# Kernel tuning notes

Measured on AMD Instinct MI355X. Metric: run time of the kernel, lower is better.

## Reference

```python
import jax, jax.numpy as jnp
import numpy as np

DEPTH, DIM, DH, H, DQ, V = 4, 1024, 4096, 8, 128, 32000
B, L = 2, 1024


def setup_inputs() -> dict:
    key = jax.random.key(0)
    ks = iter(jax.random.split(key, 48))
    def nrm(shape, scale=1.0):
        return jax.random.normal(next(ks), shape, jnp.float32) * scale
    d = {}
    d["x"] = nrm((B, L, V))
    d["tin_w"] = nrm((DIM, V), V ** -0.5)
    d["tin_b"] = nrm((DIM,), 0.02)
    d["tout_w"] = nrm((V, DIM), DIM ** -0.5)
    d["tout_b"] = nrm((V,), 0.02)
    d["wq_w"] = nrm((DEPTH, H * DQ, DIM), DIM ** -0.5)
    d["wq_b"] = nrm((DEPTH, H * DQ), 0.02)
    d["wk_w"] = nrm((DEPTH, H * DQ, DIM), DIM ** -0.5)
    d["wk_b"] = nrm((DEPTH, H * DQ), 0.02)
    d["wv_w"] = nrm((DEPTH, H * DQ, DIM), DIM ** -0.5)
    d["wv_b"] = nrm((DEPTH, H * DQ), 0.02)
    d["wo_w"] = nrm((DEPTH, DIM, H * DQ), (H * DQ) ** -0.5)
    d["wo_b"] = nrm((DEPTH, DIM), 0.02)
    d["f1_w"] = nrm((DEPTH, DH, DIM), DIM ** -0.5)
    d["f1_b"] = nrm((DEPTH, DH), 0.02)
    d["f2_w"] = nrm((DEPTH, DIM, DH), DH ** -0.5)
    d["f2_b"] = nrm((DEPTH, DIM), 0.02)
    d["phz_re"] = nrm((DEPTH, H, DQ))
    d["phz_im"] = nrm((DEPTH, H, DQ))
    d["amp"] = nrm((DEPTH, H))
    d["lc_re"] = nrm((DEPTH, H, DQ, DQ), 0.02)
    d["lc_im"] = nrm((DEPTH, H, DQ, DQ), 0.02)
    return d


def _layernorm(x):
    m = x.mean(-1, keepdims=True)
    v = ((x - m) ** 2).mean(-1, keepdims=True)
    return (x - m) * jax.lax.rsqrt(v + 1e-5)


def _retention(x, qw, qb, kw, kb, vw, vb, ow, ob, pre, pim, amp, lcr, lci):
    b, l, _ = x.shape
    q = (x @ qw.T + qb).reshape(b, l, H, DQ)
    k = (x @ kw.T + kb).reshape(b, l, H, DQ)
    v = (x @ vw.T + vb).reshape(b, l, H, DQ)
    pz = pre + 1j * pim                              # [H,DQ] complex
    phase = pz / jnp.abs(pz)                         # unit modulus
    a = jax.nn.sigmoid(amp)                          # [H]
    phazor = phase * a[:, None]
    n = jnp.arange(l)
    pp = phase[None, :, :] ** n[:, None, None]       # [L,H,DQ]
    pp_inv = phase[None, :, :] ** (-n)[:, None, None]
    php = phazor[None, :, :] ** n[:, None, None]
    lc = jax.lax.stop_gradient(lcr + 1j * lci)       # [H,DQ,DQ], detached in torch
    qc = q.astype(jnp.complex64)
    kc = k.astype(jnp.complex64)
    vc = v.astype(jnp.complex64)
    cross = jnp.einsum('blhd,lhd,hde->blhe', qc, php * phazor[None], lc)
    tril = n[:, None] >= n[None, :]
    expn = jnp.where(tril, n[:, None] - n[None, :], 0)           # [L,L]
    mask = jnp.where(tril[None], a[:, None, None] ** expn[None], 0.0)  # [H,L,L]
    qk = jnp.einsum('blhd,bmhd->bhlm', qc * pp[None], kc * pp_inv[None])
    inner = jnp.einsum('bhlm,bmhd->blhd', qk * mask[None].astype(jnp.complex64), vc)
    y = jax.nn.silu((inner + cross).real).reshape(b, l, H * DQ)
    return y @ ow.T + ob


def reference(x, tin_w, tin_b, tout_w, tout_b, wq_w, wq_b, wk_w, wk_b, wv_w, wv_b,
              wo_w, wo_b, f1_w, f1_b, f2_w, f2_b, phz_re, phz_im, amp, lc_re, lc_im):
    h = x @ tin_w.T + tin_b
    for i in range(DEPTH):
        r = _retention(_layernorm(h), wq_w[i], wq_b[i], wk_w[i], wk_b[i],
                       wv_w[i], wv_b[i], wo_w[i], wo_b[i],
                       phz_re[i], phz_im[i], amp[i], lc_re[i], lc_im[i])
        h = h + r
        f = _layernorm(h)
        f = jax.nn.silu(f @ f1_w[i].T + f1_b[i]) @ f2_w[i].T + f2_b[i]
        h = h + f
    return h @ tout_w.T + tout_b
```

## Files before the change

kernel.cpp:

```cpp
#include <hip/hip_runtime.h>
#include <hip/hip_bf16.h>
#include <stdint.h>

#define DEPTH 4
#define DIM   1024
#define DH    4096
#define NH    8
#define DQ    128
#define VOC   32000
#define BATCH 2
#define SEQ   1024
#define ROWS  (BATCH*SEQ)

#define PQKV  ((long long)ROWS*DIM)
#define PQKV3 ((long long)ROWS*3*DIM)
#define PROT  ((long long)BATCH*NH*SEQ*2*DQ)
#define PVT   ((long long)BATCH*NH*DQ*SEQ)
#define PS    ((long long)BATCH*NH*SEQ*SEQ)
#define PMID  ((long long)ROWS*DH)
#define PY    ((long long)ROWS*DIM)
#define PLC   ((long long)NH*DQ*2*DQ)

typedef __hip_bfloat16 bf16;
using f32x4  = __attribute__((ext_vector_type(4))) float;
using bf16x8 = __attribute__((ext_vector_type(8))) __bf16;

__device__ __forceinline__ void wpair(bf16* p, long long off, long long plane, float v) {
  bf16 hi = __float2bfloat16(v);
  p[off] = hi;
  p[off + plane] = __float2bfloat16(v - __bfloat162float(hi));
}

__device__ __forceinline__ void gload_lds16(const void* g, void* l) {
  __builtin_amdgcn_global_load_lds(
      (const __attribute__((address_space(1))) void*)g,
      (__attribute__((address_space(3))) void*)(uintptr_t)l,
      16, 0, 0);
}

#define BM 128
#define BN 128
#define BKK 64
#define PL 16384

template<int EPI, int SA, int SB>
__global__ __launch_bounds__(256, (SA || SB) ? 2 : 4)
void gemm_bt(const bf16* __restrict__ A, long long sA, long long pA, int lda,
             const bf16* __restrict__ B, long long sB, long long pB, int ldb, int bmod,
             void* __restrict__ Cv, long long sC, long long pC, int ldc,
             const float* __restrict__ bias, int hmod,
             int M, int N, int K, int ksplit)
{
  __shared__ int4 sbuf[1024 * (2 + SA + SB)];
  char* Asb = (char*)sbuf;
  char* Bsb = Asb + PL * (1 + SA);

  const int tid  = threadIdx.x;
  const int lane = tid & 63;
  const int wave = tid >> 6;
  const int wr   = wave >> 1;
  const int wc   = wave & 1;
  const int z    = blockIdx.z;
  const int zb   = z / ksplit;
  const int ks   = z - zb * ksplit;
  const int Kc   = K / ksplit;
  const int k0   = ks * Kc;
  const long long tm = (long long)blockIdx.x * BM;
  const long long tn = (long long)blockIdx.y * BN;

  const bf16* Ab = A + (long long)zb * sA;
  const bf16* Bb = B + (long long)(zb % bmod) * sB;

  f32x4 acc[4][4] = {};

  for (int kt = k0; kt < k0 + Kc; kt += BKK) {
#pragma unroll
    for (int j = 0; j < 4; ++j) {
      int slot0 = j*256 + wave*64;
      int i = slot0 + lane;
      int row = i >> 3;
      int gc  = (i & 7) ^ (row & 7);
      long long ga = (tm + row) * (long long)lda + kt + gc*8;
      long long gb = (tn + row) * (long long)ldb + kt + gc*8;
      gload_lds16(Ab + ga, Asb + slot0*16);
      if (SA) gload_lds16(Ab + pA + ga, Asb + PL + slot0*16);
      gload_lds16(Bb + gb, Bsb + slot0*16);
      if (SB) gload_lds16(Bb + pB + gb, Bsb + PL + slot0*16);
    }
    __syncthreads();
#pragma unroll
    for (int kh = 0; kh < 2; ++kh) {
      const int cb = kh*4 + (lane >> 4);
      int4 avh[4], bvh[4], avl[4], bvl[4];
#pragma unroll
      for (int mi = 0; mi < 4; ++mi) {
        int m = wr*64 + mi*16 + (lane & 15);
        int off = m*128 + ((cb ^ (m & 7)) << 4);
        avh[mi] = *(const int4*)(Asb + off);
        if (SA) avl[mi] = *(const int4*)(Asb + PL + off);
      }
#pragma unroll
      for (int nj = 0; nj < 4; ++nj) {
        int n = wc*64 + nj*16 + (lane & 15);
        int off = n*128 + ((cb ^ (n & 7)) << 4);
        bvh[nj] = *(const int4*)(Bsb + off);
        if (SB) bvl[nj] = *(const int4*)(Bsb + PL + off);
      }
#pragma unroll
      for (int mi = 0; mi < 4; ++mi)
#pragma unroll
        for (int nj = 0; nj < 4; ++nj)
          acc[mi][nj] = __builtin_amdgcn_mfma_f32_16x16x32_bf16(
              __builtin_bit_cast(bf16x8, avh[mi]),
              __builtin_bit_cast(bf16x8, bvh[nj]), acc[mi][nj], 0, 0, 0);
      if (SA)
#pragma unroll
        for (int mi = 0; mi < 4; ++mi)
#pragma unroll
          for (int nj = 0; nj < 4; ++nj)
            acc[mi][nj] = __builtin_amdgcn_mfma_f32_16x16x32_bf16(
                __builtin_bit_cast(bf16x8, avl[mi]),
                __builtin_bit_cast(bf16x8, bvh[nj]), acc[mi][nj], 0, 0, 0);
      if (SB)
#pragma unroll
        for (int mi = 0; mi < 4; ++mi)
#pragma unroll
          for (int nj = 0; nj < 4; ++nj)
            acc[mi][nj] = __builtin_amdgcn_mfma_f32_16x16x32_bf16(
                __builtin_bit_cast(bf16x8, avh[mi]),
                __builtin_bit_cast(bf16x8, bvl[nj]), acc[mi][nj], 0, 0, 0);
    }
    __syncthreads();
  }

  const float* dtab = (EPI == 7) ? bias + (zb % hmod) * (SEQ + 1) : nullptr;
  const int col = lane & 15;
  const int rb  = (lane >> 4) << 2;
  float* Cf = (float*)Cv + (long long)zb * sC;
  bf16*  Ch = (bf16*) Cv + (long long)zb * sC;

#pragma unroll
  for (int mi = 0; mi < 4; ++mi)
#pragma unroll
    for (int nj = 0; nj < 4; ++nj) {
      long long gn = tn + wc*64 + nj*16 + col;
      float bv_ = (EPI != 7 && bias && ks == 0) ? bias[gn] : 0.f;
#pragma unroll
      for (int r = 0; r < 4; ++r) {
        long long gm = tm + wr*64 + mi*16 + rb + r;
        float v = acc[mi][nj][r] + bv_;
        long long off = gm * (long long)ldc + gn;
        if (EPI == 0)      Cf[off] = v;
        else if (EPI == 3) { if (ksplit > 1) atomicAdd(&Cf[off], v); else Cf[off] += v; }
        else if (EPI == 5) wpair(Ch, off, pC, v);
        else if (EPI == 6) wpair(Ch, off, pC, v / (1.f + __expf(-v)));
        else {
          long long dlt = gm - gn;
          float dcy = (dlt >= 0) ? dtab[dlt] : 0.f;
          Ch[off] = __float2bfloat16(acc[mi][nj][r] * dcy);
        }
      }
    }
}

__global__ void zero_kernel(float4* __restrict__ p, long long n4) {
  long long i = (long long)blockIdx.x * blockDim.x + threadIdx.x;
  if (i < n4) p[i] = float4{0.f, 0.f, 0.f, 0.f};
}

__global__ void cast_kernel(const float* __restrict__ in,
                            bf16* __restrict__ out, long long n4) {
  long long i = (long long)blockIdx.x * blockDim.x + threadIdx.x;
  if (i >= n4) return;
  float4 v = ((const float4*)in)[i];
  bf16 a = __float2bfloat16(v.x), b = __float2bfloat16(v.y);
  bf16 c = __float2bfloat16(v.z), d = __float2bfloat16(v.w);
  ushort4 o{__builtin_bit_cast(unsigned short, a), __builtin_bit_cast(unsigned short, b),
            __builtin_bit_cast(unsigned short, c), __builtin_bit_cast(unsigned short, d)};
  ((ushort4*)out)[i] = o;
}

__global__ void cast_pair_kernel(const float* __restrict__ in,
                                 bf16* __restrict__ hi, bf16* __restrict__ lo,
                                 long long n) {
  long long i = (long long)blockIdx.x * blockDim.x + threadIdx.x;
  if (i >= n) return;
  float v = in[i];
  bf16 h = __float2bfloat16(v);
  hi[i] = h;
  lo[i] = __float2bfloat16(v - __bfloat162float(h));
}

__global__ void bias3_kernel(const float* __restrict__ q, const float* __restrict__ k,
                             const float* __restrict__ v, float* __restrict__ o) {
  int i = blockIdx.x * blockDim.x + threadIdx.x;
  if (i < DIM) o[i] = q[i];
  else if (i < 2*DIM) o[i] = k[i - DIM];
  else if (i < 3*DIM) o[i] = v[i - 2*DIM];
}

__global__ void decay_kernel(const float* __restrict__ amp, float* __restrict__ dtab) {
  const int h = blockIdx.x, n = threadIdx.x;
  const float a = 1.f / (1.f + __expf(-amp[h]));
  for (int i = n; i <= SEQ; i += blockDim.x)
    dtab[h*(SEQ+1) + i] = powf(a, (float)i);
}

__global__ void ln_kernel(const float* __restrict__ in, bf16* __restrict__ out) {
  const int row = blockIdx.x;
  const int tid = threadIdx.x;
  const float4 v = ((const float4*)(in + (size_t)row*DIM))[tid];
  float s  = v.x + v.y + v.z + v.w;
  float s2 = v.x*v.x + v.y*v.y + v.z*v.z + v.w*v.w;
#pragma unroll
  for (int o = 32; o > 0; o >>= 1) { s += __shfl_xor(s, o); s2 += __shfl_xor(s2, o); }
  __shared__ float red[8];
  const int wv = tid >> 6;
  if ((tid & 63) == 0) { red[wv] = s; red[4 + wv] = s2; }
  __syncthreads();
  s  = red[0] + red[1] + red[2] + red[3];
  s2 = red[4] + red[5] + red[6] + red[7];
  const float mean = s * (1.f / DIM);
  const float var  = s2 * (1.f / DIM) - mean * mean;
  const float inv  = rsqrtf(var + 1e-5f);
  long long base = (long long)row*DIM + tid*4;
  wpair(out, base + 0, PQKV, (v.x - mean) * inv);
  wpair(out, base + 1, PQKV, (v.y - mean) * inv);
  wpair(out, base + 2, PQKV, (v.z - mean) * inv);
  wpair(out, base + 3, PQKV, (v.w - mean) * inv);
}

__global__ void rotate_kernel(const bf16* __restrict__ qkv,
                              const float* __restrict__ pre, const float* __restrict__ pim,
                              const float* __restrict__ dtab,
                              bf16* __restrict__ qrot, bf16* __restrict__ krot,
                              bf16* __restrict__ qwb) {
  const int d = threadIdx.x, l = blockIdx.x, h = blockIdx.y, b = blockIdx.z;
  const float tr = pre[h*DQ + d], ti = pim[h*DQ + d];
  const float theta = atan2f(ti, tr);
  const long long rowb = (long long)(b*SEQ + l)*(3*DIM) + h*DQ + d;
  const float qv = __bfloat162float(qkv[rowb]) + __bfloat162float(qkv[rowb + PQKV3]);
  const float kv = __bfloat162float(qkv[rowb + DIM]) + __bfloat162float(qkv[rowb + DIM + PQKV3]);
  float sn, cs;
  sincosf(theta * (float)l, &sn, &cs);
  const long long dst = ((long long)(b*NH + h)*SEQ + l)*(2*DQ) + d;
  qrot[dst]      = __float2bfloat16(qv * cs);
  qrot[dst + DQ] = __float2bfloat16(qv * sn);
  krot[dst]      = __float2bfloat16(kv * cs);
  krot[dst + DQ] = __float2bfloat16(kv * sn);
  float sn2, cs2;
  sincosf(theta * (float)(l + 1), &sn2, &cs2);
  const float ad = dtab[h*(SEQ+1) + l + 1];
  qwb[dst]      = __float2bfloat16(qv * ad * cs2);
  qwb[dst + DQ] = __float2bfloat16(qv * ad * sn2);
}

__global__ void vt_kernel(const bf16* __restrict__ qkv, bf16* __restrict__ vt) {
  __shared__ float tile[64][65];
  const int t  = threadIdx.x;
  const int c  = t & 63, r4 = t >> 6;
  const int m0 = blockIdx.x * 64;
  const int d0 = blockIdx.y * 64;
  const int h  = blockIdx.z & (NH - 1);
  const int b  = blockIdx.z >> 3;
#pragma unroll
  for (int rr = 0; rr < 64; rr += 4) {
    const int m = m0 + rr + r4;
    const long long src = (long long)(b*SEQ + m)*(3*DIM) + 2*DIM + h*DQ + d0 + c;
    tile[rr + r4][c] = __bfloat162float(qkv[src]) + __bfloat162float(qkv[src + PQKV3]);
  }
  __syncthreads();
#pragma unroll
  for (int rr = 0; rr < 64; rr += 4) {
    const int d = rr + r4;
    vt[((long long)(b*NH + h)*DQ + d0 + d)*SEQ + m0 + c] = __float2bfloat16(tile[c][d]);
  }
}

__global__ void siluret_kernel(const float* __restrict__ ret, bf16* __restrict__ y) {
  const int d = threadIdx.x, l = blockIdx.x, h = blockIdx.y, b = blockIdx.z;
  float r = ret[((long long)(b*NH + h)*SEQ + l)*DQ + d];
  float s = r / (1.f + __expf(-r));
  wpair(y, ((long long)(b*SEQ + l)*NH + h)*DQ + d, PY, s);
}

__global__ void lccat_kernel(const float* __restrict__ lcr, const float* __restrict__ lci,
                             bf16* __restrict__ lc) {
  const int d = threadIdx.x, e = blockIdx.x, h = blockIdx.y;
  float vr = lcr[((long long)h*DQ + d)*DQ + e];
  float vi = lci[((long long)h*DQ + d)*DQ + e];
  long long dst = ((long long)h*DQ + e)*(2*DQ) + d;
  lc[dst]      = __float2bfloat16(vr);
  lc[dst + DQ] = __float2bfloat16(-vi);
}

extern "C" void kernel_launch(void* const* d_in, const int* in_sizes, int n_in,
                              void* d_out, int out_size, void* d_ws, size_t ws_size,
                              hipStream_t stream) {
  const float* x      = (const float*)d_in[0];
  const float* tin_w  = (const float*)d_in[1];
  const float* tin_b  = (const float*)d_in[2];
  const float* tout_w = (const float*)d_in[3];
  const float* tout_b = (const float*)d_in[4];
  const float* wq_w   = (const float*)d_in[5];
  const float* wq_b   = (const float*)d_in[6];
  const float* wk_w   = (const float*)d_in[7];
  const float* wk_b   = (const float*)d_in[8];
  const float* wv_w   = (const float*)d_in[9];
  const float* wv_b   = (const float*)d_in[10];
  const float* wo_w   = (const float*)d_in[11];
  const float* wo_b   = (const float*)d_in[12];
  const float* f1_w   = (const float*)d_in[13];
  const float* f1_b   = (const float*)d_in[14];
  const float* f2_w   = (const float*)d_in[15];
  const float* f2_b   = (const float*)d_in[16];
  const float* phz_re = (const float*)d_in[17];
  const float* phz_im = (const float*)d_in[18];
  const float* amp    = (const float*)d_in[19];
  const float* lc_re  = (const float*)d_in[20];
  const float* lc_im  = (const float*)d_in[21];
  (void)in_sizes; (void)n_in; (void)out_size; (void)ws_size;

  char* w = (char*)d_ws;
  auto alloc = [&](size_t bytes) {
    char* p = w; w += (bytes + 255) & ~(size_t)255; return p;
  };
  auto palloc = [&](long long elems) {
    return (bf16*)alloc((size_t)elems * 2 * 2);
  };

  const long long WP = 3LL*DIM*DIM;
  float* h     = (float*)alloc((size_t)ROWS*DIM*4);
  float* ret   = (float*)alloc((size_t)BATCH*NH*SEQ*DQ*4);
  float* qkvbi = (float*)alloc((size_t)3*DIM*4);
  float* dtab  = (float*)alloc((size_t)NH*(SEQ+1)*4);
  bf16*  hb    = palloc(PQKV);
  bf16*  Wqkv  = palloc(WP);
  bf16*  Wol   = palloc((long long)DIM*DIM);
  bf16*  Wf1l  = palloc((long long)DH*DIM);
  bf16*  Wf2l  = (bf16*)alloc((size_t)DIM*DH*2);
  bf16*  qkvb  = palloc(PQKV3);
  bf16*  lcc   = (bf16*)alloc((size_t)PLC*2);
  bf16*  Wbig  = (bf16*)alloc((size_t)DIM*VOC*2);
  bf16*  qrot  = (bf16*)alloc((size_t)PROT*2);
  bf16*  krot  = (bf16*)alloc((size_t)PROT*2);
  bf16*  qwb   = (bf16*)alloc((size_t)PROT*2);
  bf16*  vtb   = (bf16*)alloc((size_t)PVT*2);
  bf16*  Sb    = (bf16*)alloc((size_t)PS*2);
  bf16*  mid   = palloc(PMID);
  bf16*  xb = (bf16*)d_out;
  bf16*  yb = qkvb;

  auto cast = [&](const float* in, bf16* out, long long n) {
    long long n4 = n / 4;
    cast_kernel<<<dim3((unsigned)((n4 + 255) / 256)), dim3(256), 0, stream>>>(in, out, n4);
  };
  auto cast_pair = [&](const float* in, bf16* hi, bf16* lo, long long n) {
    cast_pair_kernel<<<dim3((unsigned)((n + 255) / 256)), dim3(256), 0, stream>>>(in, hi, lo, n);
  };
  auto zero = [&](float* p, long long nfloats) {
    long long n4 = nfloats / 4;
    zero_kernel<<<dim3((unsigned)((n4 + 255) / 256)), dim3(256), 0, stream>>>((float4*)p, n4);
  };

  auto gemm = [&](int epi, int sa, int sb, const bf16* A, long long sA, long long pA, int lda,
                  const bf16* B, long long sB, long long pB, int ldb, int bmod,
                  void* C, long long sC, long long pC, int ldc,
                  const float* bias, int hmod, int M, int N, int K, int batch, int ksplit) {
    dim3 g(M / BM, N / BN, batch * ksplit), blk(256);
    if (epi == 3 && !sa && !sb)      gemm_bt<3,0,0><<<g, blk, 0, stream>>>(A,sA,pA,lda,B,sB,pB,ldb,bmod,C,sC,pC,ldc,bias,hmod,M,N,K,ksplit);
    else if (epi == 7)               gemm_bt<7,0,0><<<g, blk, 0, stream>>>(A,sA,pA,lda,B,sB,pB,ldb,bmod,C,sC,pC,ldc,bias,hmod,M,N,K,ksplit);
    else if (epi == 0 && sa && !sb)  gemm_bt<0,1,0><<<g, blk, 0, stream>>>(A,sA,pA,lda,B,sB,pB,ldb,bmod,C,sC,pC,ldc,bias,hmod,M,N,K,ksplit);
    else if (epi == 3 && sa && !sb)  gemm_bt<3,1,0><<<g, blk, 0, stream>>>(A,sA,pA,lda,B,sB,pB,ldb,bmod,C,sC,pC,ldc,bias,hmod,M,N,K,ksplit);
    else if (epi == 3)               gemm_bt<3,1,1><<<g, blk, 0, stream>>>(A,sA,pA,lda,B,sB,pB,ldb,bmod,C,sC,pC,ldc,bias,hmod,M,N,K,ksplit);
    else if (epi == 5)               gemm_bt<5,1,1><<<g, blk, 0, stream>>>(A,sA,pA,lda,B,sB,pB,ldb,bmod,C,sC,pC,ldc,bias,hmod,M,N,K,ksplit);
    else if (epi == 6)               gemm_bt<6,1,1><<<g, blk, 0, stream>>>(A,sA,pA,lda,B,sB,pB,ldb,bmod,C,sC,pC,ldc,bias,hmod,M,N,K,ksplit);
  };
  const int BIG = 1 << 30;

  cast(x, xb, (long long)ROWS*VOC);
  cast(tin_w, Wbig, (long long)DIM*VOC);
  zero(h, (long long)ROWS*DIM);
  gemm(3, 0, 0, xb, 0, 0, VOC, Wbig, 0, 0, VOC, BIG, h, 0, 0, DIM, tin_b, 1,
       ROWS, DIM, VOC, 1, 10);

  for (int i = 0; i < DEPTH; ++i) {
    cast_pair(wq_w + (size_t)i*DIM*DIM, Wqkv,             Wqkv + WP,             (long long)DIM*DIM);
    cast_pair(wk_w + (size_t)i*DIM*DIM, Wqkv +   DIM*DIM, Wqkv + WP +   DIM*DIM, (long long)DIM*DIM);
    cast_pair(wv_w + (size_t)i*DIM*DIM, Wqkv + 2*DIM*DIM, Wqkv + WP + 2*DIM*DIM, (long long)DIM*DIM);
    cast_pair(wo_w + (size_t)i*DIM*DIM, Wol,  Wol  + (long long)DIM*DIM, (long long)DIM*DIM);
    cast_pair(f1_w + (size_t)i*DH*DIM,  Wf1l, Wf1l + (long long)DH*DIM,  (long long)DH*DIM);
    cast(f2_w + (size_t)i*DIM*DH, Wf2l, (long long)DIM*DH);
    bias3_kernel<<<dim3(12), dim3(256), 0, stream>>>(
        wq_b + i*DIM, wk_b + i*DIM, wv_b + i*DIM, qkvbi);
    decay_kernel<<<dim3(NH), dim3(256), 0, stream>>>(amp + i*NH, dtab);

    ln_kernel<<<ROWS, 256, 0, stream>>>(h, hb);
    gemm(5, 1, 1, hb, 0, PQKV, DIM, Wqkv, 0, WP, DIM, BIG,
         qkvb, 0, PQKV3, 3*DIM, qkvbi, 1, ROWS, 3*DIM, DIM, 1, 1);
    rotate_kernel<<<dim3(SEQ, NH, BATCH), DQ, 0, stream>>>(
        qkvb, phz_re + i*NH*DQ, phz_im + i*NH*DQ, dtab, qrot, krot, qwb);
    vt_kernel<<<dim3(SEQ/64, DQ/64, BATCH*NH), 256, 0, stream>>>(qkvb, vtb);
    lccat_kernel<<<dim3(DQ, NH), DQ, 0, stream>>>(
        lc_re + (size_t)i*NH*DQ*DQ, lc_im + (size_t)i*NH*DQ*DQ, lcc);
    gemm(7, 0, 0, qrot, (long long)SEQ*2*DQ, 0, 2*DQ,
         krot, (long long)SEQ*2*DQ, 0, 2*DQ, BIG,
         Sb, (long long)SEQ*SEQ, 0, SEQ, dtab, NH, SEQ, SEQ, 2*DQ, BATCH*NH, 1);
    zero(ret, (long long)BATCH*NH*SEQ*DQ);
    gemm(3, 0, 0, Sb, (long long)SEQ*SEQ, 0, SEQ,
         vtb, (long long)DQ*SEQ, 0, SEQ, BIG,
         ret, (long long)SEQ*DQ, 0, DQ, nullptr, 1, SEQ, DQ, SEQ, BATCH*NH, 4);
    gemm(3, 0, 0, qwb, (long long)SEQ*2*DQ, 0, 2*DQ,
         lcc, (long long)DQ*2*DQ, 0, 2*DQ, NH,
         ret, (long long)SEQ*DQ, 0, DQ, nullptr, 1, SEQ, DQ, 2*DQ, BATCH*NH, 2);
    siluret_kernel<<<dim3(SEQ, NH, BATCH), DQ, 0, stream>>>(ret, yb);
    gemm(3, 1, 1, yb, 0, PY, DIM, Wol, 0, (long long)DIM*DIM, DIM, BIG,
         h, 0, 0, DIM, wo_b + i*DIM, 1, ROWS, DIM, DIM, 1, 2);

    ln_kernel<<<ROWS, 256, 0, stream>>>(h, hb);
    gemm(6, 1, 1, hb, 0, PQKV, DIM, Wf1l, 0, (long long)DH*DIM, DIM, BIG,
         mid, 0, PMID, DH, f1_b + i*DH, 1, ROWS, DH, DIM, 1, 1);
    gemm(3, 1, 0, mid, 0, PMID, DH, Wf2l, 0, 0, DH, BIG,
         h, 0, 0, DIM, f2_b + i*DIM, 1, ROWS, DIM, DH, 1, 4);
  }

  cast_pair(h, hb, hb + PQKV, PQKV);
  cast(tout_w, Wbig, (long long)VOC*DIM);
  gemm(0, 1, 0, hb, 0, PQKV, DIM, Wbig, 0, 0, DIM, BIG,
       (float*)d_out, 0, 0, VOC, tout_b, 1, ROWS, VOC, DIM, 1, 1);
}
```

Before: 1.955 ms.

## Skip upper-triangle tiles in retention GEMMs and merge small prep kernels

Adds a causal mode to the tiled GEMM. The score GEMM skips tiles that lie entirely above the diagonal, and the score-times-V GEMM stops its K loop at the diagonal block. This removes roughly half the work in the two retention matmuls. Separately, the many small cast, zero, bias, decay and lc-concat launches are merged into a few combined elementwise kernels to cut launch overhead. Correctness depends on the unwritten upper score tiles never being read, which the truncated K range is meant to ensure.

```diff
diff --git a/kernel.cpp b/kernel.cpp
--- a/kernel.cpp
+++ b/kernel.cpp
@@ -19,7 +19,6 @@
 #define PS    ((long long)BATCH*NH*SEQ*SEQ)
 #define PMID  ((long long)ROWS*DH)
 #define PY    ((long long)ROWS*DIM)
-#define PLC   ((long long)NH*DQ*2*DQ)
 
 typedef __hip_bfloat16 bf16;
 using f32x4  = __attribute__((ext_vector_type(4))) float;
@@ -49,7 +48,7 @@
              const bf16* __restrict__ B, long long sB, long long pB, int ldb, int bmod,
              void* __restrict__ Cv, long long sC, long long pC, int ldc,
              const float* __restrict__ bias, int hmod,
-             int M, int N, int K, int ksplit)
+             int M, int N, int K, int ksplit, int causal)
 {
   __shared__ int4 sbuf[1024 * (2 + SA + SB)];
   char* Asb = (char*)sbuf;
@@ -65,23 +64,30 @@
   const int ks   = z - zb * ksplit;
   const int Kc   = K / ksplit;
   const int k0   = ks * Kc;
-  const long long tm = (long long)blockIdx.x * BM;
-  const long long tn = (long long)blockIdx.y * BN;
+  const int tm   = blockIdx.x * BM;
+  const int tn   = blockIdx.y * BN;
+
+  if (causal == 1 && tn >= tm + BM) return;
+  int kend = k0 + Kc;
+  if (causal == 2) {
+    kend = min(kend, tm + BM);
+    if (kend <= k0) return;
+  }
 
   const bf16* Ab = A + (long long)zb * sA;
   const bf16* Bb = B + (long long)(zb % bmod) * sB;
 
   f32x4 acc[4][4] = {};
 
-  for (int kt = k0; kt < k0 + Kc; kt += BKK) {
+  for (int kt = k0; kt < kend; kt += BKK) {
 #pragma unroll
     for (int j = 0; j < 4; ++j) {
       int slot0 = j*256 + wave*64;
       int i = slot0 + lane;
       int row = i >> 3;
       int gc  = (i & 7) ^ (row & 7);
-      long long ga = (tm + row) * (long long)lda + kt + gc*8;
-      long long gb = (tn + row) * (long long)ldb + kt + gc*8;
+      long long ga = (long long)(tm + row) * lda + kt + gc*8;
+      long long gb = (long long)(tn + row) * ldb + kt + gc*8;
       gload_lds16(Ab + ga, Asb + slot0*16);
       if (SA) gload_lds16(Ab + pA + ga, Asb + PL + slot0*16);
       gload_lds16(Bb + gb, Bsb + slot0*16);
@@ -163,47 +169,108 @@
     }
 }
 
-__global__ void zero_kernel(float4* __restrict__ p, long long n4) {
+__global__ void castw_kernel(const float* __restrict__ wq, const float* __restrict__ wk,
+                             const float* __restrict__ wv, const float* __restrict__ wo,
+                             const float* __restrict__ f1, const float* __restrict__ f2,
+                             bf16* __restrict__ Wqkv, bf16* __restrict__ Wol,
+                             bf16* __restrict__ Wf1, bf16* __restrict__ Wf2) {
+  const long long S1 = (long long)DIM*DIM;
+  const long long WP = 3*S1;
   long long i = (long long)blockIdx.x * blockDim.x + threadIdx.x;
-  if (i < n4) p[i] = float4{0.f, 0.f, 0.f, 0.f};
-}
-
-__global__ void cast_kernel(const float* __restrict__ in,
-                            bf16* __restrict__ out, long long n4) {
+  if (i < 3*S1) {
+    const float* src = (i < S1) ? wq : (i < 2*S1) ? wk : wv;
+    float v = src[i & (S1-1)];
+    bf16 h = __float2bfloat16(v);
+    Wqkv[i] = h;
+    Wqkv[i + WP] = __float2bfloat16(v - __bfloat162float(h));
+  } else if (i < 4*S1) {
+    long long j = i - 3*S1;
+    float v = wo[j];
+    bf16 h = __float2bfloat16(v);
+    Wol[j] = h;
+    Wol[j + S1] = __float2bfloat16(v - __bfloat162float(h));
+  } else if (i < 8*S1) {
+    long long j = i - 4*S1;
+    float v = f1[j];
+    bf16 h = __float2bfloat16(v);
+    Wf1[j] = h;
+    Wf1[j + 4*S1] = __float2bfloat16(v - __bfloat162float(h));
+  } else if (i < 12*S1) {
+    long long j = i - 8*S1;
+    Wf2[j] = __float2bfloat16(f2[j]);
+  }
+}
+
+#define MISC_LC   (NH*DQ*DQ)
+#define MISC_B3   (MISC_LC + 3*DIM)
+#define MISC_DC   (MISC_B3 + NH*(SEQ+1))
+#define MISC_ZR   (MISC_DC + (BATCH*NH*SEQ*DQ)/4)
+__global__ void misc_kernel(const float* __restrict__ lcr, const float* __restrict__ lci,
+                            bf16* __restrict__ lc,
+                            const float* __restrict__ bq, const float* __restrict__ bk,
+                            const float* __restrict__ bv, float* __restrict__ qkvbi,
+                            const float* __restrict__ amp, float* __restrict__ dtab,
+                            float4* __restrict__ retz) {
   long long i = (long long)blockIdx.x * blockDim.x + threadIdx.x;
-  if (i >= n4) return;
-  float4 v = ((const float4*)in)[i];
-  bf16 a = __float2bfloat16(v.x), b = __float2bfloat16(v.y);
-  bf16 c = __float2bfloat16(v.z), d = __float2bfloat16(v.w);
-  ushort4 o{__builtin_bit_cast(unsigned short, a), __builtin_bit_cast(unsigned short, b),
-            __builtin_bit_cast(unsigned short, c), __builtin_bit_cast(unsigned short, d)};
-  ((ushort4*)out)[i] = o;
-}
-
-__global__ void cast_pair_kernel(const float* __restrict__ in,
-                                 bf16* __restrict__ hi, bf16* __restrict__ lo,
-                                 long long n) {
+  if (i < MISC_LC) {
+    int d = i & 127, e = (i >> 7) & 127, h = i >> 14;
+    float vr = lcr[((long long)h*DQ + d)*DQ + e];
+    float vi = lci[((long long)h*DQ + d)*DQ + e];
+    long long dst = ((long long)h*DQ + e)*(2*DQ) + d;
+    lc[dst]      = __float2bfloat16(vr);
+    lc[dst + DQ] = __float2bfloat16(-vi);
+  } else if (i < MISC_B3) {
+    int j = (int)(i - MISC_LC);
+    qkvbi[j] = (j < DIM) ? bq[j] : (j < 2*DIM) ? bk[j - DIM] : bv[j - 2*DIM];
+  } else if (i < MISC_DC) {
+    int j = (int)(i - MISC_B3);
+    int h = j / (SEQ+1), n = j % (SEQ+1);
+    float a = 1.f / (1.f + __expf(-amp[h]));
+    dtab[j] = powf(a, (float)n);
+  } else if (i < MISC_ZR) {
+    retz[i - MISC_DC] = float4{0.f, 0.f, 0.f, 0.f};
+  }
+}
+
+#define TIN_X4 ((long long)ROWS*VOC/4)
+#define TIN_W4 (TIN_X4 + (long long)DIM*VOC/4)
+#define TIN_H4 (TIN_W4 + (long long)ROWS*DIM/4)
+__global__ void tinprep_kernel(const float* __restrict__ x, bf16* __restrict__ xb,
+                               const float* __restrict__ tw, bf16* __restrict__ twb,
+                               float4* __restrict__ hz) {
   long long i = (long long)blockIdx.x * blockDim.x + threadIdx.x;
-  if (i >= n) return;
-  float v = in[i];
-  bf16 h = __float2bfloat16(v);
-  hi[i] = h;
-  lo[i] = __float2bfloat16(v - __bfloat162float(h));
-}
-
-__global__ void bias3_kernel(const float* __restrict__ q, const float* __restrict__ k,
-                             const float* __restrict__ v, float* __restrict__ o) {
-  int i = blockIdx.x * blockDim.x + threadIdx.x;
-  if (i < DIM) o[i] = q[i];
-  else if (i < 2*DIM) o[i] = k[i - DIM];
-  else if (i < 3*DIM) o[i] = v[i - 2*DIM];
-}
-
-__global__ void decay_kernel(const float* __restrict__ amp, float* __restrict__ dtab) {
-  const int h = blockIdx.x, n = threadIdx.x;
-  const float a = 1.f / (1.f + __expf(-amp[h]));
-  for (int i = n; i <= SEQ; i += blockDim.x)
-    dtab[h*(SEQ+1) + i] = powf(a, (float)i);
+  const float* src; bf16* dst; long long j;
+  if (i < TIN_X4)      { src = x;  dst = xb;  j = i; }
+  else if (i < TIN_W4) { src = tw; dst = twb; j = i - TIN_X4; }
+  else if (i < TIN_H4) { hz[i - TIN_W4] = float4{0.f,0.f,0.f,0.f}; return; }
+  else return;
+  float4 v = ((const float4*)src)[j];
+  ushort4 o{__builtin_bit_cast(unsigned short, __float2bfloat16(v.x)),
+            __builtin_bit_cast(unsigned short, __float2bfloat16(v.y)),
+            __builtin_bit_cast(unsigned short, __float2bfloat16(v.z)),
+            __builtin_bit_cast(unsigned short, __float2bfloat16(v.w))};
+  ((ushort4*)dst)[j] = o;
+}
+
+#define TAIL_H (PQKV)
+#define TAIL_W (TAIL_H + (long long)VOC*DIM/4)
+__global__ void tailprep_kernel(const float* __restrict__ h, bf16* __restrict__ hb,
+                                const float* __restrict__ tw, bf16* __restrict__ twb) {
+  long long i = (long long)blockIdx.x * blockDim.x + threadIdx.x;
+  if (i < TAIL_H) {
+    float v = h[i];
+    bf16 hi = __float2bfloat16(v);
+    hb[i] = hi;
+    hb[i + PQKV] = __float2bfloat16(v - __bfloat162float(hi));
+  } else if (i < TAIL_W) {
+    long long j = i - TAIL_H;
+    float4 v = ((const float4*)tw)[j];
+    ushort4 o{__builtin_bit_cast(unsigned short, __float2bfloat16(v.x)),
+              __builtin_bit_cast(unsigned short, __float2bfloat16(v.y)),
+              __builtin_bit_cast(unsigned short, __float2bfloat16(v.z)),
+              __builtin_bit_cast(unsigned short, __float2bfloat16(v.w))};
+    ((ushort4*)twb)[j] = o;
+  }
 }
 
 __global__ void ln_kernel(const float* __restrict__ in, bf16* __restrict__ out) {
@@ -282,16 +349,6 @@
   float r = ret[((long long)(b*NH + h)*SEQ + l)*DQ + d];
   float s = r / (1.f + __expf(-r));
   wpair(y, ((long long)(b*SEQ + l)*NH + h)*DQ + d, PY, s);
-}
-
-__global__ void lccat_kernel(const float* __restrict__ lcr, const float* __restrict__ lci,
-                             bf16* __restrict__ lc) {
-  const int d = threadIdx.x, e = blockIdx.x, h = blockIdx.y;
-  float vr = lcr[((long long)h*DQ + d)*DQ + e];
-  float vi = lci[((long long)h*DQ + d)*DQ + e];
-  long long dst = ((long long)h*DQ + e)*(2*DQ) + d;
-  lc[dst]      = __float2bfloat16(vr);
-  lc[dst + DQ] = __float2bfloat16(-vi);
 }
 
 extern "C" void kernel_launch(void* const* d_in, const int* in_sizes, int n_in,
@@ -340,7 +397,7 @@
   bf16*  Wf1l  = palloc((long long)DH*DIM);
   bf16*  Wf2l  = (bf16*)alloc((size_t)DIM*DH*2);
   bf16*  qkvb  = palloc(PQKV3);
-  bf16*  lcc   = (bf16*)alloc((size_t)PLC*2);
+  bf16*  lcc   = (bf16*)alloc((size_t)NH*DQ*2*DQ*2);
   bf16*  Wbig  = (bf16*)alloc((size_t)DIM*VOC*2);
   bf16*  qrot  = (bf16*)alloc((size_t)PROT*2);
   bf16*  krot  = (bf16*)alloc((size_t)PROT*2);
@@ -351,81 +408,71 @@
   bf16*  xb = (bf16*)d_out;
   bf16*  yb = qkvb;
 
-  auto cast = [&](const float* in, bf16* out, long long n) {
-    long long n4 = n / 4;
-    cast_kernel<<<dim3((unsigned)((n4 + 255) / 256)), dim3(256), 0, stream>>>(in, out, n4);
-  };
-  auto cast_pair = [&](const float* in, bf16* hi, bf16* lo, long long n) {
-    cast_pair_kernel<<<dim3((unsigned)((n + 255) / 256)), dim3(256), 0, stream>>>(in, hi, lo, n);
-  };
-  auto zero = [&](float* p, long long nfloats) {
-    long long n4 = nfloats / 4;
-    zero_kernel<<<dim3((unsigned)((n4 + 255) / 256)), dim3(256), 0, stream>>>((float4*)p, n4);
-  };
-
   auto gemm = [&](int epi, int sa, int sb, const bf16* A, long long sA, long long pA, int lda,
                   const bf16* B, long long sB, long long pB, int ldb, int bmod,
                   void* C, long long sC, long long pC, int ldc,
-                  const float* bias, int hmod, int M, int N, int K, int batch, int ksplit) {
+                  const float* bias, int hmod, int M, int N, int K, int batch,
+                  int ksplit, int causal) {
     dim3 g(M / BM, N / BN, batch * ksplit), blk(256);
-    if (epi == 3 && !sa && !sb)      gemm_bt<3,0,0><<<g, blk, 0, stream>>>(A,sA,pA,lda,B,sB,pB,ldb,bmod,C,sC,pC,ldc,bias,hmod,M,N,K,ksplit);
-    else if (epi == 7)               gemm_bt<7,0,0><<<g, blk, 0, stream>>>(A,sA,pA,lda,B,sB,pB,ldb,bmod,C,sC,pC,ldc,bias,hmod,M,N,K,ksplit);
-    else if (epi == 0 && sa && !sb)  gemm_bt<0,1,0><<<g, blk, 0, stream>>>(A,sA,pA,lda,B,sB,pB,ldb,bmod,C,sC,pC,ldc,bias,hmod,M,N,K,ksplit);
-    else if (epi == 3 && sa && !sb)  gemm_bt<3,1,0><<<g, blk, 0, stream>>>(A,sA,pA,lda,B,sB,pB,ldb,bmod,C,sC,pC,ldc,bias,hmod,M,N,K,ksplit);
-    else if (epi == 3)               gemm_bt<3,1,1><<<g, blk, 0, stream>>>(A,sA,pA,lda,B,sB,pB,ldb,bmod,C,sC,pC,ldc,bias,hmod,M,N,K,ksplit);
-    else if (epi == 5)               gemm_bt<5,1,1><<<g, blk, 0, stream>>>(A,sA,pA,lda,B,sB,pB,ldb,bmod,C,sC,pC,ldc,bias,hmod,M,N,K,ksplit);
-    else if (epi == 6)               gemm_bt<6,1,1><<<g, blk, 0, stream>>>(A,sA,pA,lda,B,sB,pB,ldb,bmod,C,sC,pC,ldc,bias,hmod,M,N,K,ksplit);
+    if (epi == 3 && !sa && !sb)      gemm_bt<3,0,0><<<g, blk, 0, stream>>>(A,sA,pA,lda,B,sB,pB,ldb,bmod,C,sC,pC,ldc,bias,hmod,M,N,K,ksplit,causal);
+    else if (epi == 7)               gemm_bt<7,0,0><<<g, blk, 0, stream>>>(A,sA,pA,lda,B,sB,pB,ldb,bmod,C,sC,pC,ldc,bias,hmod,M,N,K,ksplit,causal);
+    else if (epi == 0 && sa && !sb)  gemm_bt<0,1,0><<<g, blk, 0, stream>>>(A,sA,pA,lda,B,sB,pB,ldb,bmod,C,sC,pC,ldc,bias,hmod,M,N,K,ksplit,causal);
+    else if (epi == 3 && sa && !sb)  gemm_bt<3,1,0><<<g, blk, 0, stream>>>(A,sA,pA,lda,B,sB,pB,ldb,bmod,C,sC,pC,ldc,bias,hmod,M,N,K,ksplit,causal);
+    else if (epi == 3)               gemm_bt<3,1,1><<<g, blk, 0, stream>>>(A,sA,pA,lda,B,sB,pB,ldb,bmod,C,sC,pC,ldc,bias,hmod,M,N,K,ksplit,causal);
+    else if (epi == 5)               gemm_bt<5,1,1><<<g, blk, 0, stream>>>(A,sA,pA,lda,B,sB,pB,ldb,bmod,C,sC,pC,ldc,bias,hmod,M,N,K,ksplit,causal);
+    else if (epi == 6)               gemm_bt<6,1,1><<<g, blk, 0, stream>>>(A,sA,pA,lda,B,sB,pB,ldb,bmod,C,sC,pC,ldc,bias,hmod,M,N,K,ksplit,causal);
   };
   const int BIG = 1 << 30;
 
-  cast(x, xb, (long long)ROWS*VOC);
-  cast(tin_w, Wbig, (long long)DIM*VOC);
-  zero(h, (long long)ROWS*DIM);
+  {
+    long long tot = TIN_H4;
+    tinprep_kernel<<<dim3((unsigned)((tot + 255) / 256)), dim3(256), 0, stream>>>(
+        x, xb, tin_w, Wbig, (float4*)h);
+  }
   gemm(3, 0, 0, xb, 0, 0, VOC, Wbig, 0, 0, VOC, BIG, h, 0, 0, DIM, tin_b, 1,
-       ROWS, DIM, VOC, 1, 10);
+       ROWS, DIM, VOC, 1, 10, 0);
 
   for (int i = 0; i < DEPTH; ++i) {
-    cast_pair(wq_w + (size_t)i*DIM*DIM, Wqkv,             Wqkv + WP,             (long long)DIM*DIM);
-    cast_pair(wk_w + (size_t)i*DIM*DIM, Wqkv +   DIM*DIM, Wqkv + WP +   DIM*DIM, (long long)DIM*DIM);
-    cast_pair(wv_w + (size_t)i*DIM*DIM, Wqkv + 2*DIM*DIM, Wqkv + WP + 2*DIM*DIM, (long long)DIM*DIM);
-    cast_pair(wo_w + (size_t)i*DIM*DIM, Wol,  Wol  + (long long)DIM*DIM, (long long)DIM*DIM);
-    cast_pair(f1_w + (size_t)i*DH*DIM,  Wf1l, Wf1l + (long long)DH*DIM,  (long long)DH*DIM);
-    cast(f2_w + (size_t)i*DIM*DH, Wf2l, (long long)DIM*DH);
-    bias3_kernel<<<dim3(12), dim3(256), 0, stream>>>(
-        wq_b + i*DIM, wk_b + i*DIM, wv_b + i*DIM, qkvbi);
-    decay_kernel<<<dim3(NH), dim3(256), 0, stream>>>(amp + i*NH, dtab);
+    {
+      long long tot = 12LL*DIM*DIM;
+      castw_kernel<<<dim3((unsigned)((tot + 255) / 256)), dim3(256), 0, stream>>>(
+          wq_w + (size_t)i*DIM*DIM, wk_w + (size_t)i*DIM*DIM, wv_w + (size_t)i*DIM*DIM,
+          wo_w + (size_t)i*DIM*DIM, f1_w + (size_t)i*DH*DIM, f2_w + (size_t)i*DIM*DH,
+          Wqkv, Wol, Wf1l, Wf2l);
+      misc_kernel<<<dim3((unsigned)((MISC_ZR + 255) / 256)), dim3(256), 0, stream>>>(
+          lc_re + (size_t)i*NH*DQ*DQ, lc_im + (size_t)i*NH*DQ*DQ, lcc,
+          wq_b + i*DIM, wk_b + i*DIM, wv_b + i*DIM, qkvbi,
+          amp + i*NH, dtab, (float4*)ret);
+    }
 
     ln_kernel<<<ROWS, 256, 0, stream>>>(h, hb);
     gemm(5, 1, 1, hb, 0, PQKV, DIM, Wqkv, 0, WP, DIM, BIG,
-         qkvb, 0, PQKV3, 3*DIM, qkvbi, 1, ROWS, 3*DIM, DIM, 1, 1);
+         qkvb, 0, PQKV3, 3*DIM, qkvbi, 1, ROWS, 3*DIM, DIM, 1, 1, 0);
     rotate_kernel<<<dim3(SEQ, NH, BATCH), DQ, 0, stream>>>(
         qkvb, phz_re + i*NH*DQ, phz_im + i*NH*DQ, dtab, qrot, krot, qwb);
     vt_kernel<<<dim3(SEQ/64, DQ/64, BATCH*NH), 256, 0, stream>>>(qkvb, vtb);
-    lccat_kernel<<<dim3(DQ, NH), DQ, 0, stream>>>(
-        lc_re + (size_t)i*NH*DQ*DQ, lc_im + (size_t)i*NH*DQ*DQ, lcc);
     gemm(7, 0, 0, qrot, (long long)SEQ*2*DQ, 0, 2*DQ,
          krot, (long long)SEQ*2*DQ, 0, 2*DQ, BIG,
-         Sb, (long long)SEQ*SEQ, 0, SEQ, dtab, NH, SEQ, SEQ, 2*DQ, BATCH*NH, 1);
-    zero(ret, (long long)BATCH*NH*SEQ*DQ);
+         Sb, (long long)SEQ*SEQ, 0, SEQ, dtab, NH, SEQ, SEQ, 2*DQ, BATCH*NH, 1, 1);
     gemm(3, 0, 0, Sb, (long long)SEQ*SEQ, 0, SEQ,
          vtb, (long long)DQ*SEQ, 0, SEQ, BIG,
-         ret, (long long)SEQ*DQ, 0, DQ, nullptr, 1, SEQ, DQ, SEQ, BATCH*NH, 4);
+         ret, (long long)SEQ*DQ, 0, DQ, nullptr, 1, SEQ, DQ, SEQ, BATCH*NH, 4, 2);
     gemm(3, 0, 0, qwb, (long long)SEQ*2*DQ, 0, 2*DQ,
          lcc, (long long)DQ*2*DQ, 0, 2*DQ, NH,
-         ret, (long long)SEQ*DQ, 0, DQ, nullptr, 1, SEQ, DQ, 2*DQ, BATCH*NH, 2);
+         ret, (long long)SEQ*DQ, 0, DQ, nullptr, 1, SEQ, DQ, 2*DQ, BATCH*NH, 2, 0);
     siluret_kernel<<<dim3(SEQ, NH, BATCH), DQ, 0, stream>>>(ret, yb);
     gemm(3, 1, 1, yb, 0, PY, DIM, Wol, 0, (long long)DIM*DIM, DIM, BIG,
-         h, 0, 0, DIM, wo_b + i*DIM, 1, ROWS, DIM, DIM, 1, 2);
+         h, 0, 0, DIM, wo_b + i*DIM, 1, ROWS, DIM, DIM, 1, 2, 0);
 
     ln_kernel<<<ROWS, 256, 0, stream>>>(h, hb);
     gemm(6, 1, 1, hb, 0, PQKV, DIM, Wf1l, 0, (long long)DH*DIM, DIM, BIG,
-         mid, 0, PMID, DH, f1_b + i*DH, 1, ROWS, DH, DIM, 1, 1);
+         mid, 0, PMID, DH, f1_b + i*DH, 1, ROWS, DH, DIM, 1, 1, 0);
     gemm(3, 1, 0, mid, 0, PMID, DH, Wf2l, 0, 0, DH, BIG,
-         h, 0, 0, DIM, f2_b + i*DIM, 1, ROWS, DIM, DH, 1, 4);
-  }
-
-  cast_pair(h, hb, hb + PQKV, PQKV);
-  cast(tout_w, Wbig, (long long)VOC*DIM);
+         h, 0, 0, DIM, f2_b + i*DIM, 1, ROWS, DIM, DH, 1, 4, 0);
+  }
+
+  tailprep_kernel<<<dim3((unsigned)((TAIL_W + 255) / 256)), dim3(256), 0, stream>>>(
+      h, hb, tout_w, Wbig);
   gemm(0, 1, 0, hb, 0, PQKV, DIM, Wbig, 0, 0, DIM, BIG,
-       (float*)d_out, 0, 0, VOC, tout_b, 1, ROWS, VOC, DIM, 1, 1);
-}
+       (float*)d_out, 0, 0, VOC, tout_b, 1, ROWS, VOC, DIM, 1, 1, 0);
+}
```

New measurement: 1.864 ms. 4.6% less time.
